# Performance work log

Hardware: AMD Instinct MI355X
Metric: run time of the kernel (lower is better)

Reference implementation:

```python
import jax, jax.numpy as jnp
import numpy as np

B, N, C = 2048, 4096, 1024
UNITS, RANK = 4096, 512


def _orth(key, shape):
    a = jax.random.normal(key, shape, dtype=jnp.float32)
    q, r = jnp.linalg.qr(a if shape[0] >= shape[1] else a.T)
    q = q * jnp.sign(jnp.diagonal(r))[None, :]
    return q if shape[0] >= shape[1] else q.T


def setup_inputs() -> dict:
    key = jax.random.key(0)
    k1, k2, k3, k4, k5, k6 = jax.random.split(key, 6)
    inputs = jax.random.normal(k1, (B, N), dtype=jnp.float32)
    context = jax.random.normal(k2, (B, C), dtype=jnp.float32)
    U = _orth(k3, (N, RANK))
    V = _orth(k4, (UNITS, RANK))
    W = _orth(k5, (C, RANK))
    # SingularValueInitializer stand-in: positive values scaled like glorot singular values
    S = jnp.abs(jax.random.normal(k6, (RANK,), dtype=jnp.float32)) * jnp.sqrt(2.0 / (N + UNITS))
    bias = jnp.zeros((UNITS,), dtype=jnp.float32)
    return {"inputs": inputs, "context": context, "U": U, "S": S, "V": V, "W": W, "bias": bias}


def reference(inputs, context, U, S, V, W, bias):
    # s_b = S + context @ W  -> per-batch singular values [B, R]
    s = S[None, :] + context @ W
    # Original: kernel_b = U diag(s_b) V^T; out_b = x_b @ kernel_b.
    # Associativity: out = ((x @ U) * s) @ V^T  -- identical math, no [B,N,M] intermediate.
    xu = inputs @ U                      # [B, R]
    out = (xu * s) @ V.T                 # [B, UNITS]
    out = out + bias[None, :]
    return jax.nn.relu(out)
```

## Files before the change

### kernel.cpp

```cpp
#include <hip/hip_runtime.h>
#include <hip/hip_bf16.h>

typedef __attribute__((ext_vector_type(8))) __bf16 bf16x8;
typedef __attribute__((ext_vector_type(4))) float f32x4;
typedef __attribute__((ext_vector_type(8))) unsigned short ushort8;
typedef __attribute__((ext_vector_type(4))) unsigned short ushort4v;

__device__ __forceinline__ unsigned short f2bf(float f) {
  unsigned u = __builtin_bit_cast(unsigned, f);
  u += 0x7FFFu + ((u >> 16) & 1u);
  return (unsigned short)(u >> 16);
}

__device__ __forceinline__ void gload_lds16(const void* g, void* l) {
  __builtin_amdgcn_global_load_lds(
      (const __attribute__((address_space(1))) void*)g,
      (__attribute__((address_space(3))) void*)l, 16, 0, 0);
}

__device__ __forceinline__ void barrier_fence() {
  __builtin_amdgcn_s_barrier();
  asm volatile("" ::: "memory");
}

__global__ __launch_bounds__(256) void prep_kernel(
    const float* __restrict__ U, unsigned short* __restrict__ Ut,
    const float* __restrict__ W, unsigned short* __restrict__ Wt,
    const float* __restrict__ V, unsigned short* __restrict__ Vb,
    const float* __restrict__ inp, unsigned short* __restrict__ inb,
    const float* __restrict__ ctx, unsigned short* __restrict__ ctxb) {
  __shared__ float tile[32][33];
  const int b = blockIdx.x;
  const int tid = threadIdx.x;
  if (b < 2560) {
    const float* src;
    unsigned short* dst;
    int rows, cols, bx, by;
    if (b < 2048) {
      src = U; dst = Ut; rows = 4096; cols = 512;
      bx = (b & 15) * 32; by = (b >> 4) * 32;
    } else {
      int bb = b - 2048;
      src = W; dst = Wt; rows = 1024; cols = 512;
      bx = (bb & 15) * 32; by = (bb >> 4) * 32;
    }
    const int tx = tid & 31, ty = tid >> 5;
    for (int i = ty; i < 32; i += 8)
      tile[i][tx] = src[(size_t)(by + i) * cols + bx + tx];
    __syncthreads();
    for (int i = ty; i < 32; i += 8)
      dst[(size_t)(bx + i) * rows + by + tx] = f2bf(tile[tx][i]);
  } else {
    const float* src;
    unsigned short* dst;
    size_t i;
    if (b < 3584)      { src = V;   dst = Vb;   i = (size_t)(b - 2560) * 256 + tid; }
    else if (b < 7680) { src = inp; dst = inb;  i = (size_t)(b - 3584) * 256 + tid; }
    else               { src = ctx; dst = ctxb; i = (size_t)(b - 7680) * 256 + tid; }
    const float4* s4 = reinterpret_cast<const float4*>(src) + 2 * i;
    float4 a = s4[0], c = s4[1];
    ushort8 o;
    o[0] = f2bf(a.x); o[1] = f2bf(a.y); o[2] = f2bf(a.z); o[3] = f2bf(a.w);
    o[4] = f2bf(c.x); o[5] = f2bf(c.y); o[6] = f2bf(c.z); o[7] = f2bf(c.w);
    *(reinterpret_cast<ushort8*>(dst) + i) = o;
  }
}

template <int EPI>
__device__ __forceinline__ void gemm_core(
    const unsigned short* __restrict__ A, const unsigned short* __restrict__ Bt,
    int N, int lda, int kchunk, int k0, const float* __restrict__ e0,
    float* __restrict__ outf, int nwg, int bid) {
  constexpr int FM = 2, FN = 4;
  constexpr int BM = 32 * FM, BN = 32 * FN, BK = 64;
  constexpr int AI = BM / 32, BI = BN / 32;
  __shared__ unsigned short lds[2][(BM + BN) * BK];

  const int tid = threadIdx.x;
  const int wid = tid >> 6;
  const int lane = tid & 63;
  const int wr = wid >> 1, wc = wid & 1;

  const int swz = (bid & 7) * (nwg >> 3) + (bid >> 3);
  const int nbn = N / BN;
  const int brow = (swz / nbn) * BM;
  const int bcol = (swz % nbn) * BN;

  f32x4 zero = {0.f, 0.f, 0.f, 0.f};
  f32x4 acc[FM][FN];
#pragma unroll
  for (int m = 0; m < FM; ++m)
#pragma unroll
    for (int n = 0; n < FN; ++n) acc[m][n] = zero;

  const int lr = lane >> 3;
  const int swzc = ((lane & 7) ^ lr) * 8;
  const unsigned short* Agh = A + (size_t)(brow + wid * (BM / 4) + lr) * lda + swzc + k0;
  const unsigned short* Bgh = Bt + (size_t)(bcol + wid * (BN / 4) + lr) * lda + swzc + k0;

  const int frow = lane & 15;
  const int fhi = lane >> 4;

  const int nsteps = kchunk / BK;

  auto stage = [&](int b, int kofs) {
    unsigned short* AsW = lds[b] + wid * (BM / 4) * 64;
#pragma unroll
    for (int i = 0; i < AI; ++i)
      gload_lds16(Agh + kofs + (size_t)i * 8 * lda, AsW + i * 512);
    unsigned short* BsW = lds[b] + BM * BK + wid * (BN / 4) * 64;
#pragma unroll
    for (int i = 0; i < BI; ++i)
      gload_lds16(Bgh + kofs + (size_t)i * 8 * lda, BsW + i * 512);
  };

  auto compute = [&](int cur) {
    const unsigned short* As = lds[cur];
    const unsigned short* Bs = lds[cur] + BM * BK;
#pragma unroll
    for (int ks = 0; ks < 2; ++ks) {
      bf16x8 af[FM], bg[FN];
#pragma unroll
      for (int m = 0; m < FM; ++m) {
        int row = wr * FM * 16 + m * 16 + frow;
        int pc = (ks * 4 + fhi) ^ (row & 7);
        af[m] = *reinterpret_cast<const bf16x8*>(As + row * 64 + pc * 8);
      }
#pragma unroll
      for (int n = 0; n < FN; ++n) {
        int row = wc * FN * 16 + n * 16 + frow;
        int pc = (ks * 4 + fhi) ^ (row & 7);
        bg[n] = *reinterpret_cast<const bf16x8*>(Bs + row * 64 + pc * 8);
      }
#pragma unroll
      for (int m = 0; m < FM; ++m)
#pragma unroll
        for (int n = 0; n < FN; ++n)
          acc[m][n] = __builtin_amdgcn_mfma_f32_16x16x32_bf16(af[m], bg[n],
                                                              acc[m][n], 0, 0, 0);
    }
  };

  stage(0, 0);
  stage(1, BK);

  int cur = 0;
  for (int t = 0; t < nsteps; ++t) {
    if (t + 1 < nsteps)
      asm volatile("s_waitcnt vmcnt(6)" ::: "memory");
    else
      asm volatile("s_waitcnt vmcnt(0)" ::: "memory");
    barrier_fence();
    compute(cur);
    if (t + 1 < nsteps) {
      asm volatile("s_waitcnt lgkmcnt(0)" ::: "memory");
      barrier_fence();
      if (t + 2 < nsteps) stage(cur, (t + 2) * BK);
    }
    cur ^= 1;
  }

#pragma unroll
  for (int m = 0; m < FM; ++m) {
    int gr0 = brow + wr * FM * 16 + m * 16 + fhi * 4;
#pragma unroll
    for (int n = 0; n < FN; ++n) {
      int gc = bcol + wc * FN * 16 + n * 16 + frow;
#pragma unroll
      for (int j = 0; j < 4; ++j) {
        size_t idx = (size_t)(gr0 + j) * N + gc;
        float v = acc[m][n][j];
        if constexpr (EPI == 2) {
          v += e0[gc];
          outf[idx] = v > 0.f ? v : 0.f;
        } else {
          outf[idx] = v;
        }
      }
    }
  }
}

__global__ __launch_bounds__(256) void gemm01_kernel(
    const unsigned short* __restrict__ inb, const unsigned short* __restrict__ Ut,
    const unsigned short* __restrict__ ctxb, const unsigned short* __restrict__ Wt,
    float* __restrict__ p0, float* __restrict__ p1) {
  const int bid = (int)blockIdx.x;
  constexpr size_t MN = (size_t)2048 * 512;
  if (bid < 512) {
    const int split = bid >> 7;
    gemm_core<3>(inb, Ut, 512, 4096, 1024, split * 1024, nullptr,
                 p1 + split * MN, 128, bid & 127);
  } else {
    const int sb = bid - 512;
    const int split = sb >> 7;
    gemm_core<3>(ctxb, Wt, 512, 1024, 512, split * 512, nullptr,
                 p0 + split * MN, 128, sb & 127);
  }
}

__global__ __launch_bounds__(256) void gemm2_kernel(
    const unsigned short* __restrict__ xus, const unsigned short* __restrict__ Vb,
    const float* __restrict__ bias, float* __restrict__ out) {
  gemm_core<2>(xus, Vb, 4096, 512, 512, 0, bias, out, 1024, (int)blockIdx.x);
}

__global__ void reduce_mul_kernel(const float* __restrict__ p1,
                                  const float* __restrict__ p0,
                                  const float* __restrict__ Svec,
                                  unsigned short* __restrict__ xus, int MN) {
  int i = blockIdx.x * blockDim.x + threadIdx.x;
  size_t base = (size_t)i * 4;
  if (base >= (size_t)MN) return;
  float4 a = *reinterpret_cast<const float4*>(p1 + base);
  float4 b = *reinterpret_cast<const float4*>(p1 + (size_t)MN + base);
  float4 c = *reinterpret_cast<const float4*>(p1 + 2 * (size_t)MN + base);
  float4 d = *reinterpret_cast<const float4*>(p1 + 3 * (size_t)MN + base);
  float4 s0 = *reinterpret_cast<const float4*>(p0 + base);
  float4 s1 = *reinterpret_cast<const float4*>(p0 + (size_t)MN + base);
  float4 sv = *reinterpret_cast<const float4*>(Svec + (base & 511));
  float4 xu, s;
  xu.x = (a.x + b.x) + (c.x + d.x);  s.x = s0.x + s1.x + sv.x;
  xu.y = (a.y + b.y) + (c.y + d.y);  s.y = s0.y + s1.y + sv.y;
  xu.z = (a.z + b.z) + (c.z + d.z);  s.z = s0.z + s1.z + sv.z;
  xu.w = (a.w + b.w) + (c.w + d.w);  s.w = s0.w + s1.w + sv.w;
  ushort4v o;
  o[0] = f2bf(xu.x * s.x);
  o[1] = f2bf(xu.y * s.y);
  o[2] = f2bf(xu.z * s.z);
  o[3] = f2bf(xu.w * s.w);
  *reinterpret_cast<ushort4v*>(xus + base) = o;
}

extern "C" void kernel_launch(void* const* d_in, const int* in_sizes, int n_in,
                              void* d_out, int out_size, void* d_ws, size_t ws_size,
                              hipStream_t stream) {
  constexpr int Bm = 2048, Nn = 4096, Cc = 1024, UU = 4096, RR = 512;
  const float* inputs  = (const float*)d_in[0];
  const float* context = (const float*)d_in[1];
  const float* U       = (const float*)d_in[2];
  const float* S       = (const float*)d_in[3];
  const float* V       = (const float*)d_in[4];
  const float* W       = (const float*)d_in[5];
  const float* bias    = (const float*)d_in[6];
  float* out = (float*)d_out;

  char* p = (char*)d_ws;
  unsigned short* Ut   = (unsigned short*)p; p += (size_t)RR * Nn * 2;
  unsigned short* Wt   = (unsigned short*)p; p += (size_t)RR * Cc * 2;
  unsigned short* Vb   = (unsigned short*)p; p += (size_t)UU * RR * 2;
  unsigned short* inb  = (unsigned short*)p; p += (size_t)Bm * Nn * 2;
  unsigned short* ctxb = (unsigned short*)p; p += (size_t)Bm * Cc * 2;
  float*          p0   = (float*)p;          p += (size_t)2 * Bm * RR * 4;
  float*          p1   = (float*)p;          p += (size_t)4 * Bm * RR * 4;
  unsigned short* xus  = (unsigned short*)p; p += (size_t)Bm * RR * 2;

  prep_kernel<<<8704, 256, 0, stream>>>(U, Ut, W, Wt, V, Vb, inputs, inb,
                                        context, ctxb);

  gemm01_kernel<<<768, 256, 0, stream>>>(inb, Ut, ctxb, Wt, p0, p1);

  reduce_mul_kernel<<<Bm * RR / 4 / 256, 256, 0, stream>>>(p1, p0, S, xus, Bm * RR);

  gemm2_kernel<<<1024, 256, 0, stream>>>(xus, Vb, bias, out);
}
```

Baseline: 59.39 us.

## Load fp32 activations directly in GEMM and convert to bf16 in registers

Drops the prep pass that converted inputs and context to bf16 in global memory. The first GEMM now streams fp32 A tiles into swizzled LDS and converts them to bf16 while building MFMA fragments. This removes one full write and re-read of the largest activation tensors. In exchange the A tile doubles in LDS footprint and global load traffic, and the compute loop does extra LDS reads and conversions.

New measurement: 58.25 us. Within noise of the previous version (-1.9%).

```diff
diff --git a/kernel.cpp b/kernel.cpp
--- a/kernel.cpp
+++ b/kernel.cpp
@@ -23,12 +23,17 @@
   asm volatile("" ::: "memory");
 }
 
+template <int N>
+__device__ __forceinline__ void waitvm() {
+  if constexpr (N == 0)      asm volatile("s_waitcnt vmcnt(0)" ::: "memory");
+  else if constexpr (N == 6) asm volatile("s_waitcnt vmcnt(6)" ::: "memory");
+  else if constexpr (N == 8) asm volatile("s_waitcnt vmcnt(8)" ::: "memory");
+}
+
 __global__ __launch_bounds__(256) void prep_kernel(
     const float* __restrict__ U, unsigned short* __restrict__ Ut,
     const float* __restrict__ W, unsigned short* __restrict__ Wt,
-    const float* __restrict__ V, unsigned short* __restrict__ Vb,
-    const float* __restrict__ inp, unsigned short* __restrict__ inb,
-    const float* __restrict__ ctx, unsigned short* __restrict__ ctxb) {
+    const float* __restrict__ V, unsigned short* __restrict__ Vb) {
   __shared__ float tile[32][33];
   const int b = blockIdx.x;
   const int tid = threadIdx.x;
@@ -51,30 +56,28 @@
     for (int i = ty; i < 32; i += 8)
       dst[(size_t)(bx + i) * rows + by + tx] = f2bf(tile[tx][i]);
   } else {
-    const float* src;
-    unsigned short* dst;
-    size_t i;
-    if (b < 3584)      { src = V;   dst = Vb;   i = (size_t)(b - 2560) * 256 + tid; }
-    else if (b < 7680) { src = inp; dst = inb;  i = (size_t)(b - 3584) * 256 + tid; }
-    else               { src = ctx; dst = ctxb; i = (size_t)(b - 7680) * 256 + tid; }
-    const float4* s4 = reinterpret_cast<const float4*>(src) + 2 * i;
+    const size_t i = (size_t)(b - 2560) * 256 + tid;
+    const float4* s4 = reinterpret_cast<const float4*>(V) + 2 * i;
     float4 a = s4[0], c = s4[1];
     ushort8 o;
     o[0] = f2bf(a.x); o[1] = f2bf(a.y); o[2] = f2bf(a.z); o[3] = f2bf(a.w);
     o[4] = f2bf(c.x); o[5] = f2bf(c.y); o[6] = f2bf(c.z); o[7] = f2bf(c.w);
-    *(reinterpret_cast<ushort8*>(dst) + i) = o;
-  }
-}
-
-template <int EPI>
+    *(reinterpret_cast<ushort8*>(Vb) + i) = o;
+  }
+}
+
+template <int EPI, bool AF32>
 __device__ __forceinline__ void gemm_core(
-    const unsigned short* __restrict__ A, const unsigned short* __restrict__ Bt,
+    const void* __restrict__ Av, const unsigned short* __restrict__ Bt,
     int N, int lda, int kchunk, int k0, const float* __restrict__ e0,
     float* __restrict__ outf, int nwg, int bid) {
   constexpr int FM = 2, FN = 4;
   constexpr int BM = 32 * FM, BN = 32 * FN, BK = 64;
-  constexpr int AI = BM / 32, BI = BN / 32;
-  __shared__ unsigned short lds[2][(BM + BN) * BK];
+  constexpr int ABYTES = BM * BK * (AF32 ? 4 : 2);
+  constexpr int AI = AF32 ? 4 : 2;
+  constexpr int BI = 4;
+  constexpr int ISS = AI + BI;
+  __shared__ __align__(16) char lds[2][ABYTES + BN * BK * 2];
 
   const int tid = threadIdx.x;
   const int wid = tid >> 6;
@@ -95,8 +98,16 @@
 
   const int lr = lane >> 3;
   const int swzc = ((lane & 7) ^ lr) * 8;
-  const unsigned short* Agh = A + (size_t)(brow + wid * (BM / 4) + lr) * lda + swzc + k0;
-  const unsigned short* Bgh = Bt + (size_t)(bcol + wid * (BN / 4) + lr) * lda + swzc + k0;
+  const int a4r = lane >> 4;
+  const int a4c = lane & 15;
+  const int colE = ((a4c ^ a4r) << 2);
+  const int colO = ((a4c ^ (4 + a4r)) << 2);
+
+  const float* Agf =
+      (const float*)Av + (size_t)(brow + wid * 16 + a4r) * lda + k0;
+  const unsigned short* Agh =
+      (const unsigned short*)Av + (size_t)(brow + wid * 16 + lr) * lda + swzc + k0;
+  const unsigned short* Bgh = Bt + (size_t)(bcol + wid * 32 + lr) * lda + swzc + k0;
 
   const int frow = lane & 15;
   const int fhi = lane >> 4;
@@ -104,33 +115,54 @@
   const int nsteps = kchunk / BK;
 
   auto stage = [&](int b, int kofs) {
-    unsigned short* AsW = lds[b] + wid * (BM / 4) * 64;
-#pragma unroll
-    for (int i = 0; i < AI; ++i)
-      gload_lds16(Agh + kofs + (size_t)i * 8 * lda, AsW + i * 512);
-    unsigned short* BsW = lds[b] + BM * BK + wid * (BN / 4) * 64;
+    char* dstA = lds[b] + wid * (AF32 ? 4096 : 2048);
+    if constexpr (AF32) {
+#pragma unroll
+      for (int i = 0; i < 4; ++i)
+        gload_lds16(Agf + kofs + (size_t)(4 * i) * lda + ((i & 1) ? colO : colE),
+                    dstA + i * 1024);
+    } else {
+#pragma unroll
+      for (int i = 0; i < 2; ++i)
+        gload_lds16(Agh + kofs + (size_t)(8 * i) * lda, dstA + i * 1024);
+    }
+    char* dstB = lds[b] + ABYTES + wid * 4096;
 #pragma unroll
     for (int i = 0; i < BI; ++i)
-      gload_lds16(Bgh + kofs + (size_t)i * 8 * lda, BsW + i * 512);
+      gload_lds16(Bgh + kofs + (size_t)(8 * i) * lda, dstB + i * 1024);
   };
 
   auto compute = [&](int cur) {
-    const unsigned short* As = lds[cur];
-    const unsigned short* Bs = lds[cur] + BM * BK;
+    const char* base = lds[cur];
+    const unsigned short* Bs = (const unsigned short*)(base + ABYTES);
 #pragma unroll
     for (int ks = 0; ks < 2; ++ks) {
       bf16x8 af[FM], bg[FN];
 #pragma unroll
       for (int m = 0; m < FM; ++m) {
         int row = wr * FM * 16 + m * 16 + frow;
-        int pc = (ks * 4 + fhi) ^ (row & 7);
-        af[m] = *reinterpret_cast<const bf16x8*>(As + row * 64 + pc * 8);
+        int j = ks * 4 + fhi;
+        if constexpr (AF32) {
+          const float* ap = (const float*)base + row * 64;
+          int r7 = row & 7;
+          float4 lo = *(const float4*)(ap + (((2 * j) ^ r7) << 2));
+          float4 hi = *(const float4*)(ap + (((2 * j + 1) ^ r7) << 2));
+          bf16x8 tv;
+          tv[0] = (__bf16)lo.x; tv[1] = (__bf16)lo.y;
+          tv[2] = (__bf16)lo.z; tv[3] = (__bf16)lo.w;
+          tv[4] = (__bf16)hi.x; tv[5] = (__bf16)hi.y;
+          tv[6] = (__bf16)hi.z; tv[7] = (__bf16)hi.w;
+          af[m] = tv;
+        } else {
+          int pc = j ^ (row & 7);
+          af[m] = *(const bf16x8*)((const unsigned short*)base + row * 64 + pc * 8);
+        }
       }
 #pragma unroll
       for (int n = 0; n < FN; ++n) {
         int row = wc * FN * 16 + n * 16 + frow;
         int pc = (ks * 4 + fhi) ^ (row & 7);
-        bg[n] = *reinterpret_cast<const bf16x8*>(Bs + row * 64 + pc * 8);
+        bg[n] = *(const bf16x8*)(Bs + row * 64 + pc * 8);
       }
 #pragma unroll
       for (int m = 0; m < FM; ++m)
@@ -147,9 +179,9 @@
   int cur = 0;
   for (int t = 0; t < nsteps; ++t) {
     if (t + 1 < nsteps)
-      asm volatile("s_waitcnt vmcnt(6)" ::: "memory");
+      waitvm<ISS>();
     else
-      asm volatile("s_waitcnt vmcnt(0)" ::: "memory");
+      waitvm<0>();
     barrier_fence();
     compute(cur);
     if (t + 1 < nsteps) {
@@ -182,27 +214,28 @@
 }
 
 __global__ __launch_bounds__(256) void gemm01_kernel(
-    const unsigned short* __restrict__ inb, const unsigned short* __restrict__ Ut,
-    const unsigned short* __restrict__ ctxb, const unsigned short* __restrict__ Wt,
+    const float* __restrict__ inp, const unsigned short* __restrict__ Ut,
+    const float* __restrict__ ctx, const unsigned short* __restrict__ Wt,
     float* __restrict__ p0, float* __restrict__ p1) {
   const int bid = (int)blockIdx.x;
   constexpr size_t MN = (size_t)2048 * 512;
   if (bid < 512) {
     const int split = bid >> 7;
-    gemm_core<3>(inb, Ut, 512, 4096, 1024, split * 1024, nullptr,
-                 p1 + split * MN, 128, bid & 127);
+    gemm_core<3, true>(inp, Ut, 512, 4096, 1024, split * 1024, nullptr,
+                       p1 + split * MN, 128, bid & 127);
   } else {
     const int sb = bid - 512;
     const int split = sb >> 7;
-    gemm_core<3>(ctxb, Wt, 512, 1024, 512, split * 512, nullptr,
-                 p0 + split * MN, 128, sb & 127);
+    gemm_core<3, true>(ctx, Wt, 512, 1024, 512, split * 512, nullptr,
+                       p0 + split * MN, 128, sb & 127);
   }
 }
 
 __global__ __launch_bounds__(256) void gemm2_kernel(
     const unsigned short* __restrict__ xus, const unsigned short* __restrict__ Vb,
     const float* __restrict__ bias, float* __restrict__ out) {
-  gemm_core<2>(xus, Vb, 4096, 512, 512, 0, bias, out, 1024, (int)blockIdx.x);
+  gemm_core<2, false>(xus, Vb, 4096, 512, 512, 0, bias, out, 1024,
+                      (int)blockIdx.x);
 }
 
 __global__ void reduce_mul_kernel(const float* __restrict__ p1,
@@ -249,16 +282,13 @@
   unsigned short* Ut   = (unsigned short*)p; p += (size_t)RR * Nn * 2;
   unsigned short* Wt   = (unsigned short*)p; p += (size_t)RR * Cc * 2;
   unsigned short* Vb   = (unsigned short*)p; p += (size_t)UU * RR * 2;
-  unsigned short* inb  = (unsigned short*)p; p += (size_t)Bm * Nn * 2;
-  unsigned short* ctxb = (unsigned short*)p; p += (size_t)Bm * Cc * 2;
   float*          p0   = (float*)p;          p += (size_t)2 * Bm * RR * 4;
   float*          p1   = (float*)p;          p += (size_t)4 * Bm * RR * 4;
   unsigned short* xus  = (unsigned short*)p; p += (size_t)Bm * RR * 2;
 
-  prep_kernel<<<8704, 256, 0, stream>>>(U, Ut, W, Wt, V, Vb, inputs, inb,
-                                        context, ctxb);
-
-  gemm01_kernel<<<768, 256, 0, stream>>>(inb, Ut, ctxb, Wt, p0, p1);
+  prep_kernel<<<3584, 256, 0, stream>>>(U, Ut, W, Wt, V, Vb);
+
+  gemm01_kernel<<<768, 256, 0, stream>>>(inputs, Ut, context, Wt, p0, p1);
 
   reduce_mul_kernel<<<Bm * RR / 4 / 256, 256, 0, stream>>>(p1, p0, S, xus, Bm * RR);
 
```
